# Performance work log

Measured on AMD Instinct MI355X. Metric: run time of the kernel, lower is better.

The kernel has to match this reference:

```python
import jax, jax.numpy as jnp
import numpy as np

N_CLUSTERS = 131072
N_CENTROIDS = 256
D_FEAT = 64
N_BATCH = 8
COORD_RANGE = 128


def setup_inputs() -> dict:
    key = jax.random.key(0)
    k1, k2, k3, k4, k5, k6 = jax.random.split(key, 6)
    # coords: column 0 = batch index, columns 1:4 = integer xyz voxel coords
    clu_batch = jax.random.randint(k1, (N_CLUSTERS, 1), 0, N_BATCH, dtype=jnp.int32)
    clu_xyz = jax.random.randint(k2, (N_CLUSTERS, 3), 0, COORD_RANGE, dtype=jnp.int32)
    cluster_coords = jnp.concatenate([clu_batch, clu_xyz], axis=1)
    # guarantee every batch has >= 1 centroid (avoids empty-softmax rows)
    cen_batch = (jnp.arange(N_CENTROIDS, dtype=jnp.int32) % N_BATCH)[:, None]
    cen_xyz = jax.random.randint(k3, (N_CENTROIDS, 3), 0, COORD_RANGE, dtype=jnp.int32)
    centroid_coords = jnp.concatenate([cen_batch, cen_xyz], axis=1)
    cluster_feats = jax.random.normal(k4, (N_CLUSTERS, D_FEAT), dtype=jnp.float32)
    centroid_feats = jax.random.normal(k5, (N_CENTROIDS, D_FEAT), dtype=jnp.float32)
    return {
        "cluster_coords": cluster_coords,
        "cluster_feats": cluster_feats,
        "centroid_coords": centroid_coords,
        "centroid_feats": centroid_feats,
    }


def reference(cluster_coords, cluster_feats, centroid_coords, centroid_feats):
    # Per-batch pairwise-distance softmax attention, matmul, scatter into dense
    # [N, M] output filled with -inf for cross-batch pairs. Vectorized form of
    # the original python loop over batch indices: since each (cluster, centroid)
    # pair is touched only when batches match, a batch-equality mask + masked
    # softmax reproduces the per-batch math exactly.
    same_batch = cluster_coords[:, 0][:, None] == centroid_coords[:, 0][None, :]  # [N, M]

    # distances from integer xyz coords (no_grad in original -> stop_gradient, and
    # coords are ints anyway)
    diff = (cluster_coords[:, None, 1:] - centroid_coords[None, :, 1:]).astype(cluster_feats.dtype)  # [N, M, 3]
    dists = jnp.maximum(jnp.sqrt(jnp.sum(diff * diff, axis=-1)), 0.1)  # clamp(min=0.1)
    logits = jnp.where(same_batch, -dists, -jnp.inf)
    attn = jax.lax.stop_gradient(jax.nn.softmax(logits, axis=-1))  # [N, M], per-batch softmax

    scores = jnp.clip(cluster_feats @ centroid_feats.T * attn, -10.0, 10.0)  # [N, M]
    out = jnp.where(same_batch, scores, -jnp.inf)
    return out
```

## Files before the change

### kernel.cpp

```cpp
#include <hip/hip_runtime.h>

constexpr int N_CLUSTERS   = 131072;
constexpr int N_CENTROIDS  = 256;
constexpr int D_FEAT       = 64;

constexpr int THREADS        = 256;
constexpr int ROWS_PER_BLOCK = 64;

#define MASK_VAL (-1.0e30f)

typedef __attribute__((ext_vector_type(8))) short bf16x8;
typedef __attribute__((ext_vector_type(4))) float f32x4;

static __device__ inline unsigned f2bf(float f) {
    unsigned u = __float_as_uint(f);
    return (u + 0x7FFFu + ((u >> 16) & 1u)) >> 16;
}
static __device__ inline unsigned pk2(float a, float b) {
    return f2bf(a) | (f2bf(b) << 16);
}

__global__ __launch_bounds__(THREADS, 4)
void instance_head_kernel(const int*   __restrict__ clu_coords,
                          const float* __restrict__ clu_feats,
                          const int*   __restrict__ cen_coords,
                          const float* __restrict__ cen_feats,
                          float*       __restrict__ out)
{
    __shared__ unsigned Bl[(16 * 2 * 64) * 4];
    __shared__ unsigned pcc[N_CENTROIDS];
    __shared__ float    inv_l[ROWS_PER_BLOCK];

    const int t     = threadIdx.x;
    const int lane  = t & 63;
    const int wave  = __builtin_amdgcn_readfirstlane(t >> 6);
    const int m     = lane & 15;
    const int quad  = lane >> 4;
    const int r_blk = blockIdx.x * ROWS_PER_BLOCK;
    const int r0w   = r_blk + wave * 16;

    const float* aptr = clu_feats + (size_t)(r0w + m) * D_FEAT + quad * 8;
    const float4 aL0 = *(const float4*)(aptr);
    const float4 aH0 = *(const float4*)(aptr + 4);
    const float4 aL1 = *(const float4*)(aptr + 32);
    const float4 aH1 = *(const float4*)(aptr + 36);

    int4 rc[4];
    #pragma unroll
    for (int i = 0; i < 4; ++i)
        rc[i] = ((const int4*)clu_coords)[r0w + quad * 4 + i];

    #pragma unroll
    for (int i = 0; i < 8; ++i) {
        const int q = t + i * THREADS;
        const int n = q >> 3, o = q & 7;
        const float4 g0 = ((const float4*)cen_feats)[q * 2];
        const float4 g1 = ((const float4*)cen_feats)[q * 2 + 1];
        uint4 d;
        d.x = pk2(g0.x, g0.y); d.y = pk2(g0.z, g0.w);
        d.z = pk2(g1.x, g1.y); d.w = pk2(g1.z, g1.w);
        const int dst = (((n >> 4) * 2 + (o >> 2)) * 64) + (n & 15) + (o & 3) * 16;
        ((uint4*)Bl)[dst] = d;
    }
    {
        const int4 c = ((const int4*)cen_coords)[t];
        pcc[t] = (unsigned)c.x | ((unsigned)c.y << 8) |
                 ((unsigned)c.z << 16) | ((unsigned)c.w << 24);
    }
    __syncthreads();

    {
        const int rl  = t >> 2;
        const int sub = t & 3;
        const int4 ra = ((const int4*)clu_coords)[r_blk + rl];
        float sum = 0.f;
        for (int jj = 0; jj < 64; ++jj) {
            const int col = sub * 64 + ((jj + sub * 16) & 63);
            const unsigned p = pcc[col];
            const int cb = p & 0xFF;
            const int dx = ra.y - (int)((p >> 8) & 0xFF);
            const int dy = ra.z - (int)((p >> 16) & 0xFF);
            const int dz = ra.w - (int)(p >> 24);
            const float d2   = (float)(dx * dx + dy * dy + dz * dz);
            const float dist = fmaxf(__builtin_sqrtf(d2), 0.1f);
            const float u    = __expf(-dist);
            sum += (ra.x == cb) ? u : 0.f;
        }
        sum += __shfl_xor(sum, 1, 64);
        sum += __shfl_xor(sum, 2, 64);
        if (sub == 0) inv_l[rl] = (sum > 0.f) ? (1.0f / sum) : 0.f;
    }

    union { uint4 u; bf16x8 v; } a0, a1;
    a0.u.x = pk2(aL0.x, aL0.y); a0.u.y = pk2(aL0.z, aL0.w);
    a0.u.z = pk2(aH0.x, aH0.y); a0.u.w = pk2(aH0.z, aH0.w);
    a1.u.x = pk2(aL1.x, aL1.y); a1.u.y = pk2(aL1.z, aL1.w);
    a1.u.z = pk2(aH1.x, aH1.y); a1.u.w = pk2(aH1.z, aH1.w);

    __syncthreads();

    const float4 iv = *(const float4*)&inv_l[wave * 16 + quad * 4];
    const float invs[4] = {iv.x, iv.y, iv.z, iv.w};

    #pragma unroll
    for (int tt = 0; tt < 16; ++tt) {
        const bf16x8 b0 = *(const bf16x8*)&Bl[((tt * 2 + 0) * 64 + lane) * 4];
        const bf16x8 b1 = *(const bf16x8*)&Bl[((tt * 2 + 1) * 64 + lane) * 4];
        f32x4 acc = {0.f, 0.f, 0.f, 0.f};
        acc = __builtin_amdgcn_mfma_f32_16x16x32_bf16(a0.v, b0, acc, 0, 0, 0);
        acc = __builtin_amdgcn_mfma_f32_16x16x32_bf16(a1.v, b1, acc, 0, 0, 0);

        const unsigned p = pcc[tt * 16 + m];
        const int cb = p & 0xFF;
        const int cx = (p >> 8) & 0xFF, cy = (p >> 16) & 0xFF, cz = p >> 24;
        #pragma unroll
        for (int i = 0; i < 4; ++i) {
            const int dx = rc[i].y - cx, dy = rc[i].z - cy, dz = rc[i].w - cz;
            const float d2   = (float)(dx * dx + dy * dy + dz * dz);
            const float dist = fmaxf(__builtin_sqrtf(d2), 0.1f);
            const float attn = __expf(-dist) * invs[i];
            float v = acc[i] * attn;
            v = fminf(fmaxf(v, -10.f), 10.f);
            v = (rc[i].x == cb) ? v : MASK_VAL;
            out[(size_t)(r0w + quad * 4 + i) * N_CENTROIDS + tt * 16 + m] = v;
        }
    }
}

extern "C" void kernel_launch(void* const* d_in, const int* in_sizes, int n_in,
                              void* d_out, int out_size, void* d_ws, size_t ws_size,
                              hipStream_t stream) {
    const int*   clu_coords = (const int*)  d_in[0];
    const float* clu_feats  = (const float*)d_in[1];
    const int*   cen_coords = (const int*)  d_in[2];
    const float* cen_feats  = (const float*)d_in[3];
    float* out = (float*)d_out;

    dim3 grid(N_CLUSTERS / ROWS_PER_BLOCK);
    dim3 block(THREADS);
    instance_head_kernel<<<grid, block, 0, stream>>>(
        clu_coords, clu_feats, cen_coords, cen_feats, out);
}
```

Baseline: 200.3 us.

## Compute softmax weights once in registers, permute centroid columns for float4 stores

Drops the separate row-sum pass by computing the exp weights per lane once. They are cached as packed bf16 in registers, reduced across lanes with shuffles, and reused in the MFMA epilogue, so the exp/sqrt work is no longer done twice. Centroid features and coordinates are permuted in LDS so each lane owns 16 contiguous output columns, which allows float4 global stores instead of scalar ones. The LDS writes use an XOR swizzle to reduce bank conflicts. The trade-offs are more register pressure and attention weights rounded to bf16 precision, which may affect accuracy.

```diff
diff --git a/kernel.cpp b/kernel.cpp
--- a/kernel.cpp
+++ b/kernel.cpp
@@ -27,28 +27,21 @@
                           const float* __restrict__ cen_feats,
                           float*       __restrict__ out)
 {
-    __shared__ unsigned Bl[(16 * 2 * 64) * 4];
-    __shared__ unsigned pcc[N_CENTROIDS];
-    __shared__ float    inv_l[ROWS_PER_BLOCK];
+    __shared__ unsigned Bl[16 * 2 * 64 * 4];
+    __shared__ unsigned pccT[N_CENTROIDS];
 
-    const int t     = threadIdx.x;
-    const int lane  = t & 63;
-    const int wave  = __builtin_amdgcn_readfirstlane(t >> 6);
-    const int m     = lane & 15;
-    const int quad  = lane >> 4;
-    const int r_blk = blockIdx.x * ROWS_PER_BLOCK;
-    const int r0w   = r_blk + wave * 16;
+    const int t    = threadIdx.x;
+    const int lane = t & 63;
+    const int wave = __builtin_amdgcn_readfirstlane(t >> 6);
+    const int m    = lane & 15;
+    const int quad = lane >> 4;
+    const int r0w  = blockIdx.x * ROWS_PER_BLOCK + wave * 16;
 
     const float* aptr = clu_feats + (size_t)(r0w + m) * D_FEAT + quad * 8;
     const float4 aL0 = *(const float4*)(aptr);
     const float4 aH0 = *(const float4*)(aptr + 4);
     const float4 aL1 = *(const float4*)(aptr + 32);
     const float4 aH1 = *(const float4*)(aptr + 36);
-
-    int4 rc[4];
-    #pragma unroll
-    for (int i = 0; i < 4; ++i)
-        rc[i] = ((const int4*)clu_coords)[r0w + quad * 4 + i];
 
     #pragma unroll
     for (int i = 0; i < 8; ++i) {
@@ -59,36 +52,25 @@
         uint4 d;
         d.x = pk2(g0.x, g0.y); d.y = pk2(g0.z, g0.w);
         d.z = pk2(g1.x, g1.y); d.w = pk2(g1.z, g1.w);
-        const int dst = (((n >> 4) * 2 + (o >> 2)) * 64) + (n & 15) + (o & 3) * 16;
-        ((uint4*)Bl)[dst] = d;
+        const int tile = n & 15;
+        const int np   = n >> 4;
+        const int f    = o >> 2;
+        const int lp   = (np | ((o & 3) << 4)) ^ o;
+        ((uint4*)Bl)[(tile * 2 + f) * 64 + lp] = d;
     }
     {
         const int4 c = ((const int4*)cen_coords)[t];
-        pcc[t] = (unsigned)c.x | ((unsigned)c.y << 8) |
-                 ((unsigned)c.z << 16) | ((unsigned)c.w << 24);
+        pccT[((t & 15) << 4) | (t >> 4)] =
+            (unsigned)c.x | ((unsigned)c.y << 8) | ((unsigned)c.z << 16) | ((unsigned)c.w << 24);
     }
-    __syncthreads();
 
-    {
-        const int rl  = t >> 2;
-        const int sub = t & 3;
-        const int4 ra = ((const int4*)clu_coords)[r_blk + rl];
-        float sum = 0.f;
-        for (int jj = 0; jj < 64; ++jj) {
-            const int col = sub * 64 + ((jj + sub * 16) & 63);
-            const unsigned p = pcc[col];
-            const int cb = p & 0xFF;
-            const int dx = ra.y - (int)((p >> 8) & 0xFF);
-            const int dy = ra.z - (int)((p >> 16) & 0xFF);
-            const int dz = ra.w - (int)(p >> 24);
-            const float d2   = (float)(dx * dx + dy * dy + dz * dz);
-            const float dist = fmaxf(__builtin_sqrtf(d2), 0.1f);
-            const float u    = __expf(-dist);
-            sum += (ra.x == cb) ? u : 0.f;
-        }
-        sum += __shfl_xor(sum, 1, 64);
-        sum += __shfl_xor(sum, 2, 64);
-        if (sub == 0) inv_l[rl] = (sum > 0.f) ? (1.0f / sum) : 0.f;
+    int   rb[4];
+    float fx[4], fy[4], fz[4];
+    #pragma unroll
+    for (int i = 0; i < 4; ++i) {
+        const int4 rc = ((const int4*)clu_coords)[r0w + quad * 4 + i];
+        rb[i] = rc.x;
+        fx[i] = (float)rc.y; fy[i] = (float)rc.z; fz[i] = (float)rc.w;
     }
 
     union { uint4 u; bf16x8 v; } a0, a1;
@@ -99,31 +81,71 @@
 
     __syncthreads();
 
-    const float4 iv = *(const float4*)&inv_l[wave * 16 + quad * 4];
-    const float invs[4] = {iv.x, iv.y, iv.z, iv.w};
+    unsigned u01[16], u23[16];
+    float rsum[4] = {0.f, 0.f, 0.f, 0.f};
+    #pragma unroll
+    for (int tt = 0; tt < 16; ++tt) {
+        const unsigned p = pccT[tt * 16 + m];
+        const int   cb = (int)(p & 0xFF);
+        const float cx = (float)((p >> 8) & 0xFF);
+        const float cy = (float)((p >> 16) & 0xFF);
+        const float cz = (float)(p >> 24);
+        float uu[4];
+        #pragma unroll
+        for (int i = 0; i < 4; ++i) {
+            const float dx = fx[i] - cx, dy = fy[i] - cy, dz = fz[i] - cz;
+            const float d2   = fmaf(dx, dx, fmaf(dy, dy, dz * dz));
+            const float dist = fmaxf(__builtin_sqrtf(d2), 0.1f);
+            const float e    = __expf(-dist);
+            const bool  same = (rb[i] == cb);
+            rsum[i] += same ? e : 0.f;
+            uu[i]    = same ? e : -1.0f;
+        }
+        u01[tt] = pk2(uu[0], uu[1]);
+        u23[tt] = pk2(uu[2], uu[3]);
+    }
+    #pragma unroll
+    for (int s = 1; s < 16; s <<= 1) {
+        #pragma unroll
+        for (int i = 0; i < 4; ++i)
+            rsum[i] += __shfl_xor(rsum[i], s, 64);
+    }
+    float inv[4];
+    #pragma unroll
+    for (int i = 0; i < 4; ++i)
+        inv[i] = (rsum[i] > 1e-37f) ? __builtin_amdgcn_rcpf(rsum[i]) : 0.f;
+
+    const int sl0 = lane ^ (quad & 3);
+    const int sl1 = sl0 ^ 4;
+    float* obase = out + (size_t)(r0w + quad * 4) * N_CENTROIDS + m * 16;
 
     #pragma unroll
-    for (int tt = 0; tt < 16; ++tt) {
-        const bf16x8 b0 = *(const bf16x8*)&Bl[((tt * 2 + 0) * 64 + lane) * 4];
-        const bf16x8 b1 = *(const bf16x8*)&Bl[((tt * 2 + 1) * 64 + lane) * 4];
-        f32x4 acc = {0.f, 0.f, 0.f, 0.f};
-        acc = __builtin_amdgcn_mfma_f32_16x16x32_bf16(a0.v, b0, acc, 0, 0, 0);
-        acc = __builtin_amdgcn_mfma_f32_16x16x32_bf16(a1.v, b1, acc, 0, 0, 0);
+    for (int g = 0; g < 4; ++g) {
+        float v[4][4];
+        #pragma unroll
+        for (int tg = 0; tg < 4; ++tg) {
+            const int tt = g * 4 + tg;
+            const bf16x8 b0 = *(const bf16x8*)&Bl[((tt * 2 + 0) * 64 + sl0) * 4];
+            const bf16x8 b1 = *(const bf16x8*)&Bl[((tt * 2 + 1) * 64 + sl1) * 4];
+            f32x4 acc = {0.f, 0.f, 0.f, 0.f};
+            acc = __builtin_amdgcn_mfma_f32_16x16x32_bf16(a0.v, b0, acc, 0, 0, 0);
+            acc = __builtin_amdgcn_mfma_f32_16x16x32_bf16(a1.v, b1, acc, 0, 0, 0);
 
-        const unsigned p = pcc[tt * 16 + m];
-        const int cb = p & 0xFF;
-        const int cx = (p >> 8) & 0xFF, cy = (p >> 16) & 0xFF, cz = p >> 24;
+            float uu[4];
+            uu[0] = __uint_as_float(u01[tt] << 16);
+            uu[1] = __uint_as_float(u01[tt] & 0xFFFF0000u);
+            uu[2] = __uint_as_float(u23[tt] << 16);
+            uu[3] = __uint_as_float(u23[tt] & 0xFFFF0000u);
+            #pragma unroll
+            for (int i = 0; i < 4; ++i) {
+                float w = acc[i] * (fmaxf(uu[i], 0.f) * inv[i]);
+                w = fminf(fmaxf(w, -10.f), 10.f);
+                v[i][tg] = (uu[i] < 0.f) ? MASK_VAL : w;
+            }
+        }
         #pragma unroll
-        for (int i = 0; i < 4; ++i) {
-            const int dx = rc[i].y - cx, dy = rc[i].z - cy, dz = rc[i].w - cz;
-            const float d2   = (float)(dx * dx + dy * dy + dz * dz);
-            const float dist = fmaxf(__builtin_sqrtf(d2), 0.1f);
-            const float attn = __expf(-dist) * invs[i];
-            float v = acc[i] * attn;
-            v = fminf(fmaxf(v, -10.f), 10.f);
-            v = (rc[i].x == cb) ? v : MASK_VAL;
-            out[(size_t)(r0w + quad * 4 + i) * N_CENTROIDS + tt * 16 + m] = v;
-        }
+        for (int i = 0; i < 4; ++i)
+            *(float4*)(obase + (size_t)i * N_CENTROIDS + g * 4) = *(float4*)v[i];
     }
 }
 
```

Result: slower. 264.6 us (+32.1%).
